# Optimization experiments

Hardware: AMD Instinct MI355X
Metric: run time of the kernel (lower is better)

## Reference

```python
import jax, jax.numpy as jnp
import numpy as np

N_NODES = 20000
DEG = 16          # neighbors per node
IN_F = 256
HEADS = 8
D_HEAD = 64       # out_features per head


def setup_inputs() -> dict:
    key = jax.random.key(0)
    k1, k2, k3 = jax.random.split(key, 3)
    x = jax.random.normal(k1, (N_NODES, IN_F), dtype=jnp.float32)
    # xavier-ish scale for params
    W = jax.random.normal(k2, (IN_F, HEADS * D_HEAD), dtype=jnp.float32) * (2.0 / (IN_F + HEADS * D_HEAD)) ** 0.5
    a = jax.random.normal(k3, (1, HEADS, 2 * D_HEAD), dtype=jnp.float32) * 0.1
    # structured edges: each node i has DEG distinct neighbors (i + j*37) % N
    # distinctness per (row, col) pair mirrors the dense attention[row, col] = e overwrite semantics
    row = jnp.repeat(jnp.arange(N_NODES, dtype=jnp.int64), DEG)
    offs = jnp.arange(1, DEG + 1, dtype=jnp.int64) * 37
    col = (row + jnp.tile(offs, N_NODES)) % N_NODES
    edge_index = jnp.stack([row, col], axis=0)
    return {"x": x, "W": W, "a": a, "edge_index": edge_index}


def _gat_forward(x, W, a, edge_index):
    N = x.shape[0]
    H = a.shape[1]
    D = a.shape[2] // 2
    h = (x @ W).reshape(N, H, D)                         # [N, H, D]
    a_src, a_dst = a[0, :, :D], a[0, :, D:]              # [H, D] each
    # e_ij = a . cat(h_i, h_j)  decomposed into per-node terms (same math)
    alpha_src = jnp.einsum('nhd,hd->nh', h, a_src)       # [N, H]
    alpha_dst = jnp.einsum('nhd,hd->nh', h, a_dst)       # [N, H]
    row, col = edge_index[0], edge_index[1]
    e = alpha_src[row] + alpha_dst[col]                  # [E, H] edge logits
    # faithful dense softmax over dim=1 of an [N, N, H] tensor whose non-edge
    # entries are 0: denominator includes (N - deg) * exp(0 - m)
    deg = jax.ops.segment_sum(jnp.ones_like(row, dtype=x.dtype), row, num_segments=N)  # [N]
    m_edge = jax.ops.segment_max(e, row, num_segments=N)                               # [N, H]
    m = jnp.maximum(m_edge, 0.0)                         # zeros participate in the max
    exp_e = jnp.exp(e - m[row])                          # [E, H]
    denom = jax.ops.segment_sum(exp_e, row, num_segments=N) \
        + (jnp.asarray(N, x.dtype) - deg)[:, None] * jnp.exp(-m)  # [N, H]
    attn = exp_e / denom[row]                            # [E, H]
    # weighted neighbor aggregation (scatter-add over destination row)
    msgs = attn[:, :, None] * h[col]                     # [E, H, D]
    out = jax.ops.segment_sum(msgs, row, num_segments=N) # [N, H, D]
    out = jax.nn.relu(out)
    return out.reshape(N, H * D)                         # concat=True


def reference(x, W, a, edge_index):
    return _gat_forward(x, W, a, edge_index)
```

## Files before the change

kernel.cpp:

```cpp
#include <hip/hip_runtime.h>
#include <hip/hip_bf16.h>

#define N_NODES 20000
#define DEG     16
#define IN_F    256
#define HEADS   8
#define D_HEAD  64
#define OUT_F   512

typedef __attribute__((ext_vector_type(8))) short bf16x8;
typedef __attribute__((ext_vector_type(4))) float f32x4;

static __device__ __forceinline__ unsigned short f2bf(float f) {
    unsigned int u = __float_as_uint(f);
    return (unsigned short)((u + 0x7fffu + ((u >> 16) & 1u)) >> 16);
}
static __device__ __forceinline__ float bf2f(unsigned short u) {
    return __uint_as_float(((unsigned int)u) << 16);
}
static __device__ __forceinline__ unsigned int pack2(float lo, float hi) {
    return (unsigned int)f2bf(lo) | ((unsigned int)f2bf(hi) << 16);
}

__global__ __launch_bounds__(256) void wconvert(const float* __restrict__ W,
                                                unsigned short* __restrict__ Wt) {
    const int k0 = blockIdx.x * 64, c0 = blockIdx.y * 64;
    const int t = threadIdx.x;
    __shared__ unsigned short lt[64][72];
    #pragma unroll
    for (int p = 0; p < 4; ++p) {
        const int r  = (t >> 4) + p * 16;
        const int cq = (t & 15) * 4;
        float4 v = *(const float4*)(W + (size_t)(k0 + r) * OUT_F + c0 + cq);
        lt[cq + 0][r] = f2bf(v.x);
        lt[cq + 1][r] = f2bf(v.y);
        lt[cq + 2][r] = f2bf(v.z);
        lt[cq + 3][r] = f2bf(v.w);
    }
    __syncthreads();
    const int c = t >> 2, q = t & 3;
    uint4 o0 = *(const uint4*)&lt[c][q * 16];
    uint4 o1 = *(const uint4*)&lt[c][q * 16 + 8];
    unsigned short* dst = Wt + (size_t)(c0 + c) * IN_F + k0 + q * 16;
    *(uint4*)dst = o0;
    *(uint4*)(dst + 8) = o1;
}

__global__ __launch_bounds__(256) void gat_gemm_mfma(
    const float* __restrict__ x, const unsigned short* __restrict__ Wt,
    const float* __restrict__ a, unsigned short* __restrict__ hbf,
    float* __restrict__ asrc, float* __restrict__ adst)
{
    int b = blockIdx.x;
    {
        const int q = 626 / 8, r = 626 % 8;
        const int xcd = b & 7, lo = b >> 3;
        b = (xcd < r ? xcd * (q + 1) : r * (q + 1) + (xcd - r) * q) + lo;
    }
    const int bx = b & 1, by = b >> 1;
    const int row0 = by * 64, col0 = bx * 256;
    const int t = threadIdx.x, w = t >> 6, l = t & 63;
    const int lr = l & 15, lk = l >> 4;
    const int head = bx * 4 + w;
    const int wcol = col0 + w * 64;

    __shared__ unsigned short xl[2][64][40];

    f32x4 acc[4][4];
    #pragma unroll
    for (int m = 0; m < 4; ++m)
        #pragma unroll
        for (int n = 0; n < 4; ++n) acc[m][n] = (f32x4)0.f;

    const int sr = t >> 2;
    const int sq = t & 3;
    const float* xrow = x + (size_t)(row0 + sr) * IN_F + sq * 8;
    const bool rok = (row0 + sr) < N_NODES;

    {
        float4 v1 = make_float4(0.f,0.f,0.f,0.f), v2 = v1;
        if (rok) { v1 = *(const float4*)xrow; v2 = *(const float4*)(xrow + 4); }
        uint4 u;
        u.x = pack2(v1.x, v1.y); u.y = pack2(v1.z, v1.w);
        u.z = pack2(v2.x, v2.y); u.w = pack2(v2.z, v2.w);
        *(uint4*)&xl[0][sr][sq * 8] = u;
    }
    __syncthreads();

    #pragma unroll 2
    for (int kt = 0; kt < 8; ++kt) {
        const int cur = kt & 1;
        float4 v1, v2;
        if (kt < 7) {
            v1 = make_float4(0.f,0.f,0.f,0.f); v2 = v1;
            if (rok) {
                v1 = *(const float4*)(xrow + (kt + 1) * 32);
                v2 = *(const float4*)(xrow + (kt + 1) * 32 + 4);
            }
        }
        bf16x8 bfrag[4], afrag[4];
        #pragma unroll
        for (int n = 0; n < 4; ++n)
            bfrag[n] = *(const bf16x8*)(Wt + (size_t)(wcol + n * 16 + lr) * IN_F
                                        + kt * 32 + lk * 8);
        #pragma unroll
        for (int m = 0; m < 4; ++m)
            afrag[m] = *(const bf16x8*)&xl[cur][m * 16 + lr][lk * 8];
        #pragma unroll
        for (int m = 0; m < 4; ++m)
            #pragma unroll
            for (int n = 0; n < 4; ++n)
                acc[m][n] = __builtin_amdgcn_mfma_f32_16x16x32_bf16(
                                afrag[m], bfrag[n], acc[m][n], 0, 0, 0);
        if (kt < 7) {
            uint4 u;
            u.x = pack2(v1.x, v1.y); u.y = pack2(v1.z, v1.w);
            u.z = pack2(v2.x, v2.y); u.w = pack2(v2.z, v2.w);
            *(uint4*)&xl[cur ^ 1][sr][sq * 8] = u;
        }
        __syncthreads();
    }

    float avs[4], avd[4];
    #pragma unroll
    for (int n = 0; n < 4; ++n) {
        avs[n] = a[head * 128 + n * 16 + lr];
        avd[n] = a[head * 128 + 64 + n * 16 + lr];
    }
    float ps[4][4], pd[4][4];
    #pragma unroll
    for (int m = 0; m < 4; ++m)
        #pragma unroll
        for (int i = 0; i < 4; ++i) {
            float s = 0.f, d = 0.f;
            #pragma unroll
            for (int n = 0; n < 4; ++n) {
                s = fmaf(acc[m][n][i], avs[n], s);
                d = fmaf(acc[m][n][i], avd[n], d);
            }
            ps[m][i] = s; pd[m][i] = d;
        }
    #pragma unroll
    for (int m = 0; m < 4; ++m)
        #pragma unroll
        for (int i = 0; i < 4; ++i) {
            const int row = row0 + m * 16 + lk * 4 + i;
            if (row < N_NODES) {
                #pragma unroll
                for (int n = 0; n < 4; ++n)
                    hbf[(size_t)row * OUT_F + wcol + n * 16 + lr] =
                        f2bf(acc[m][n][i]);
            }
        }
    #pragma unroll
    for (int mask = 1; mask < 16; mask <<= 1)
        #pragma unroll
        for (int m = 0; m < 4; ++m)
            #pragma unroll
            for (int i = 0; i < 4; ++i) {
                ps[m][i] += __shfl_xor(ps[m][i], mask);
                pd[m][i] += __shfl_xor(pd[m][i], mask);
            }
    if (lr == 0) {
        #pragma unroll
        for (int m = 0; m < 4; ++m)
            #pragma unroll
            for (int i = 0; i < 4; ++i) {
                const int row = row0 + m * 16 + lk * 4 + i;
                if (row < N_NODES) {
                    asrc[(size_t)row * HEADS + head] = ps[m][i];
                    adst[(size_t)row * HEADS + head] = pd[m][i];
                }
            }
    }
}

__global__ __launch_bounds__(256) void gat_aggregate(
    const unsigned short* __restrict__ hbf,
    const float* __restrict__ asrc, const float* __restrict__ adst,
    const int* __restrict__ col, float* __restrict__ out)
{
    int b = blockIdx.x;
    b = (b & 7) * 625 + (b >> 3);
    const int wv = threadIdx.x >> 6, l = threadIdx.x & 63;
    const int n = b * 4 + wv;
    const int j = l & 15, h0 = l >> 4;

    const int cj = col[n * DEG + j];
    const float e0 = asrc[n * HEADS + h0]     + adst[(size_t)cj * HEADS + h0];
    const float e1 = asrc[n * HEADS + h0 + 4] + adst[(size_t)cj * HEADS + h0 + 4];

    float m0 = e0, m1 = e1;
    #pragma unroll
    for (int mask = 1; mask < 16; mask <<= 1) {
        m0 = fmaxf(m0, __shfl_xor(m0, mask));
        m1 = fmaxf(m1, __shfl_xor(m1, mask));
    }
    m0 = fmaxf(m0, 0.f); m1 = fmaxf(m1, 0.f);
    const float x0 = __expf(e0 - m0), x1 = __expf(e1 - m1);
    float s0 = x0, s1 = x1;
    #pragma unroll
    for (int mask = 1; mask < 16; mask <<= 1) {
        s0 += __shfl_xor(s0, mask);
        s1 += __shfl_xor(s1, mask);
    }
    s0 += (float)(N_NODES - DEG) * __expf(-m0);
    s1 += (float)(N_NODES - DEG) * __expf(-m1);
    const float at0 = x0 / s0, at1 = x1 / s1;

    const int hme = l >> 3;
    const int slb = (hme & 3) << 4;
    const unsigned short* hbase = hbf + (size_t)l * 8;
    float a8[8];
    #pragma unroll
    for (int q = 0; q < 8; ++q) a8[q] = 0.f;
    #pragma unroll
    for (int jj = 0; jj < DEG; ++jj) {
        const int   cjj = __shfl(cj, jj);
        const float w0  = __shfl(at0, slb | jj);
        const float w1  = __shfl(at1, slb | jj);
        const float wgt = (hme < 4) ? w0 : w1;
        const uint4 v = *(const uint4*)(hbase + (size_t)cjj * OUT_F);
        a8[0] = fmaf(wgt, bf2f((unsigned short)(v.x & 0xffffu)), a8[0]);
        a8[1] = fmaf(wgt, bf2f((unsigned short)(v.x >> 16)),     a8[1]);
        a8[2] = fmaf(wgt, bf2f((unsigned short)(v.y & 0xffffu)), a8[2]);
        a8[3] = fmaf(wgt, bf2f((unsigned short)(v.y >> 16)),     a8[3]);
        a8[4] = fmaf(wgt, bf2f((unsigned short)(v.z & 0xffffu)), a8[4]);
        a8[5] = fmaf(wgt, bf2f((unsigned short)(v.z >> 16)),     a8[5]);
        a8[6] = fmaf(wgt, bf2f((unsigned short)(v.w & 0xffffu)), a8[6]);
        a8[7] = fmaf(wgt, bf2f((unsigned short)(v.w >> 16)),     a8[7]);
    }
    float4 o0, o1;
    o0.x = fmaxf(a8[0], 0.f); o0.y = fmaxf(a8[1], 0.f);
    o0.z = fmaxf(a8[2], 0.f); o0.w = fmaxf(a8[3], 0.f);
    o1.x = fmaxf(a8[4], 0.f); o1.y = fmaxf(a8[5], 0.f);
    o1.z = fmaxf(a8[6], 0.f); o1.w = fmaxf(a8[7], 0.f);
    float* op = out + (size_t)n * OUT_F + l * 8;
    *(float4*)op = o0;
    *(float4*)(op + 4) = o1;
}

extern "C" void kernel_launch(void* const* d_in, const int* in_sizes, int n_in,
                              void* d_out, int out_size, void* d_ws, size_t ws_size,
                              hipStream_t stream) {
    const float* x  = (const float*)d_in[0];
    const float* W  = (const float*)d_in[1];
    const float* a  = (const float*)d_in[2];
    const int*   ei = (const int*)d_in[3];
    const int*   colIdx = ei + (size_t)N_NODES * DEG;
    float* out = (float*)d_out;

    unsigned char* ws = (unsigned char*)d_ws;
    unsigned short* Wt  = (unsigned short*)ws;
    unsigned short* hbf = (unsigned short*)(ws + 256 * 1024);
    float* asrc = (float*)(ws + 256 * 1024 + (size_t)N_NODES * OUT_F * 2);
    float* adst = asrc + (size_t)N_NODES * HEADS;

    wconvert<<<dim3(IN_F / 64, OUT_F / 64), 256, 0, stream>>>(W, Wt);
    gat_gemm_mfma<<<626, 256, 0, stream>>>(x, Wt, a, hbf, asrc, adst);
    gat_aggregate<<<5000, 256, 0, stream>>>(hbf, asrc, adst, colIdx, out);
}
```

Before: 130.7 us.

## Widen GEMM blocks to all heads, prefetch W fragments, batch gather loads in aggregate

The GEMM kernel now uses 512-thread blocks covering all 8 heads for 64 rows, so each x tile is loaded and converted once instead of twice, and B fragments are register-prefetched one k-step ahead. The aggregate kernel has every lane load all 16 neighbor indices and issue all 16 row gathers up front, computing softmax per lane redundantly instead of through shuffles. Normalization is deferred to a single multiply at the end, and bf16 unpacking uses cheaper mask ops. This raises register pressure (16 uint4 plus weights per lane) and duplicates exp work across lanes in exchange for more memory-level parallelism.

```diff
diff --git a/kernel.cpp b/kernel.cpp
--- a/kernel.cpp
+++ b/kernel.cpp
@@ -15,8 +15,11 @@
     unsigned int u = __float_as_uint(f);
     return (unsigned short)((u + 0x7fffu + ((u >> 16) & 1u)) >> 16);
 }
-static __device__ __forceinline__ float bf2f(unsigned short u) {
-    return __uint_as_float(((unsigned int)u) << 16);
+static __device__ __forceinline__ float bf2f_lo(unsigned int v) {
+    return __uint_as_float(v << 16);
+}
+static __device__ __forceinline__ float bf2f_hi(unsigned int v) {
+    return __uint_as_float(v & 0xffff0000u);
 }
 static __device__ __forceinline__ unsigned int pack2(float lo, float hi) {
     return (unsigned int)f2bf(lo) | ((unsigned int)f2bf(hi) << 16);
@@ -46,23 +49,16 @@
     *(uint4*)(dst + 8) = o1;
 }
 
-__global__ __launch_bounds__(256) void gat_gemm_mfma(
+__global__ __launch_bounds__(512) void gat_gemm_mfma(
     const float* __restrict__ x, const unsigned short* __restrict__ Wt,
     const float* __restrict__ a, unsigned short* __restrict__ hbf,
     float* __restrict__ asrc, float* __restrict__ adst)
 {
-    int b = blockIdx.x;
-    {
-        const int q = 626 / 8, r = 626 % 8;
-        const int xcd = b & 7, lo = b >> 3;
-        b = (xcd < r ? xcd * (q + 1) : r * (q + 1) + (xcd - r) * q) + lo;
-    }
-    const int bx = b & 1, by = b >> 1;
-    const int row0 = by * 64, col0 = bx * 256;
+    const int row0 = blockIdx.x * 64;
     const int t = threadIdx.x, w = t >> 6, l = t & 63;
     const int lr = l & 15, lk = l >> 4;
-    const int head = bx * 4 + w;
-    const int wcol = col0 + w * 64;
+    const int head = w;
+    const int wcol = w * 64;
 
     __shared__ unsigned short xl[2][64][40];
 
@@ -72,37 +68,39 @@
         #pragma unroll
         for (int n = 0; n < 4; ++n) acc[m][n] = (f32x4)0.f;
 
-    const int sr = t >> 2;
-    const int sq = t & 3;
-    const float* xrow = x + (size_t)(row0 + sr) * IN_F + sq * 8;
+    const int sr = t >> 3;
+    const int sq = t & 7;
+    const float* xrow = x + (size_t)(row0 + sr) * IN_F + sq * 4;
     const bool rok = (row0 + sr) < N_NODES;
 
     {
-        float4 v1 = make_float4(0.f,0.f,0.f,0.f), v2 = v1;
-        if (rok) { v1 = *(const float4*)xrow; v2 = *(const float4*)(xrow + 4); }
-        uint4 u;
-        u.x = pack2(v1.x, v1.y); u.y = pack2(v1.z, v1.w);
-        u.z = pack2(v2.x, v2.y); u.w = pack2(v2.z, v2.w);
-        *(uint4*)&xl[0][sr][sq * 8] = u;
-    }
+        float4 v = make_float4(0.f, 0.f, 0.f, 0.f);
+        if (rok) v = *(const float4*)xrow;
+        uint2 u;
+        u.x = pack2(v.x, v.y); u.y = pack2(v.z, v.w);
+        *(uint2*)&xl[0][sr][sq * 4] = u;
+    }
+    const unsigned short* wbase = Wt + (size_t)(wcol + lr) * IN_F + lk * 8;
+    bf16x8 bcur[4];
+    #pragma unroll
+    for (int n = 0; n < 4; ++n)
+        bcur[n] = *(const bf16x8*)(wbase + (size_t)n * 16 * IN_F);
     __syncthreads();
 
     #pragma unroll 2
     for (int kt = 0; kt < 8; ++kt) {
         const int cur = kt & 1;
-        float4 v1, v2;
+        float4 v;
+        bf16x8 bnext[4];
         if (kt < 7) {
-            v1 = make_float4(0.f,0.f,0.f,0.f); v2 = v1;
-            if (rok) {
-                v1 = *(const float4*)(xrow + (kt + 1) * 32);
-                v2 = *(const float4*)(xrow + (kt + 1) * 32 + 4);
-            }
-        }
-        bf16x8 bfrag[4], afrag[4];
-        #pragma unroll
-        for (int n = 0; n < 4; ++n)
-            bfrag[n] = *(const bf16x8*)(Wt + (size_t)(wcol + n * 16 + lr) * IN_F
-                                        + kt * 32 + lk * 8);
+            v = make_float4(0.f, 0.f, 0.f, 0.f);
+            if (rok) v = *(const float4*)(xrow + (kt + 1) * 32);
+            #pragma unroll
+            for (int n = 0; n < 4; ++n)
+                bnext[n] = *(const bf16x8*)(wbase + (size_t)n * 16 * IN_F
+                                            + (kt + 1) * 32);
+        }
+        bf16x8 afrag[4];
         #pragma unroll
         for (int m = 0; m < 4; ++m)
             afrag[m] = *(const bf16x8*)&xl[cur][m * 16 + lr][lk * 8];
@@ -111,12 +109,13 @@
             #pragma unroll
             for (int n = 0; n < 4; ++n)
                 acc[m][n] = __builtin_amdgcn_mfma_f32_16x16x32_bf16(
-                                afrag[m], bfrag[n], acc[m][n], 0, 0, 0);
+                                afrag[m], bcur[n], acc[m][n], 0, 0, 0);
         if (kt < 7) {
-            uint4 u;
-            u.x = pack2(v1.x, v1.y); u.y = pack2(v1.z, v1.w);
-            u.z = pack2(v2.x, v2.y); u.w = pack2(v2.z, v2.w);
-            *(uint4*)&xl[cur ^ 1][sr][sq * 8] = u;
+            uint2 u;
+            u.x = pack2(v.x, v.y); u.y = pack2(v.z, v.w);
+            *(uint2*)&xl[cur ^ 1][sr][sq * 4] = u;
+            #pragma unroll
+            for (int n = 0; n < 4; ++n) bcur[n] = bnext[n];
         }
         __syncthreads();
     }
@@ -182,59 +181,67 @@
 {
     int b = blockIdx.x;
     b = (b & 7) * 625 + (b >> 3);
-    const int wv = threadIdx.x >> 6, l = threadIdx.x & 63;
-    const int n = b * 4 + wv;
-    const int j = l & 15, h0 = l >> 4;
-
-    const int cj = col[n * DEG + j];
-    const float e0 = asrc[n * HEADS + h0]     + adst[(size_t)cj * HEADS + h0];
-    const float e1 = asrc[n * HEADS + h0 + 4] + adst[(size_t)cj * HEADS + h0 + 4];
-
-    float m0 = e0, m1 = e1;
-    #pragma unroll
-    for (int mask = 1; mask < 16; mask <<= 1) {
-        m0 = fmaxf(m0, __shfl_xor(m0, mask));
-        m1 = fmaxf(m1, __shfl_xor(m1, mask));
-    }
-    m0 = fmaxf(m0, 0.f); m1 = fmaxf(m1, 0.f);
-    const float x0 = __expf(e0 - m0), x1 = __expf(e1 - m1);
-    float s0 = x0, s1 = x1;
-    #pragma unroll
-    for (int mask = 1; mask < 16; mask <<= 1) {
-        s0 += __shfl_xor(s0, mask);
-        s1 += __shfl_xor(s1, mask);
-    }
-    s0 += (float)(N_NODES - DEG) * __expf(-m0);
-    s1 += (float)(N_NODES - DEG) * __expf(-m1);
-    const float at0 = x0 / s0, at1 = x1 / s1;
+    const int wv = __builtin_amdgcn_readfirstlane((int)(threadIdx.x >> 6));
+    const int l  = threadIdx.x & 63;
+    const int n  = b * 4 + wv;
+
+    int sc[DEG];
+    {
+        const int4* cp = (const int4*)(col + (size_t)n * DEG);
+        #pragma unroll
+        for (int q = 0; q < 4; ++q) {
+            int4 c4 = cp[q];
+            sc[q * 4 + 0] = c4.x; sc[q * 4 + 1] = c4.y;
+            sc[q * 4 + 2] = c4.z; sc[q * 4 + 3] = c4.w;
+        }
+    }
+
+    const unsigned short* hb = hbf + (size_t)l * 8;
+    uint4 hv[DEG];
+    #pragma unroll
+    for (int jj = 0; jj < DEG; ++jj)
+        hv[jj] = *(const uint4*)(hb + (size_t)sc[jj] * OUT_F);
 
     const int hme = l >> 3;
-    const int slb = (hme & 3) << 4;
-    const unsigned short* hbase = hbf + (size_t)l * 8;
+    const float as_n = asrc[(size_t)n * HEADS + hme];
+    float e[DEG];
+    #pragma unroll
+    for (int jj = 0; jj < DEG; ++jj)
+        e[jj] = as_n + adst[(size_t)sc[jj] * HEADS + hme];
+
+    float m = 0.f;
+    #pragma unroll
+    for (int jj = 0; jj < DEG; ++jj) m = fmaxf(m, e[jj]);
+    float wgt[DEG];
+    float s = (float)(N_NODES - DEG) * __expf(-m);
+    #pragma unroll
+    for (int jj = 0; jj < DEG; ++jj) {
+        wgt[jj] = __expf(e[jj] - m);
+        s += wgt[jj];
+    }
+    const float sinv = 1.0f / s;
+
     float a8[8];
     #pragma unroll
     for (int q = 0; q < 8; ++q) a8[q] = 0.f;
     #pragma unroll
     for (int jj = 0; jj < DEG; ++jj) {
-        const int   cjj = __shfl(cj, jj);
-        const float w0  = __shfl(at0, slb | jj);
-        const float w1  = __shfl(at1, slb | jj);
-        const float wgt = (hme < 4) ? w0 : w1;
-        const uint4 v = *(const uint4*)(hbase + (size_t)cjj * OUT_F);
-        a8[0] = fmaf(wgt, bf2f((unsigned short)(v.x & 0xffffu)), a8[0]);
-        a8[1] = fmaf(wgt, bf2f((unsigned short)(v.x >> 16)),     a8[1]);
-        a8[2] = fmaf(wgt, bf2f((unsigned short)(v.y & 0xffffu)), a8[2]);
-        a8[3] = fmaf(wgt, bf2f((unsigned short)(v.y >> 16)),     a8[3]);
-        a8[4] = fmaf(wgt, bf2f((unsigned short)(v.z & 0xffffu)), a8[4]);
-        a8[5] = fmaf(wgt, bf2f((unsigned short)(v.z >> 16)),     a8[5]);
-        a8[6] = fmaf(wgt, bf2f((unsigned short)(v.w & 0xffffu)), a8[6]);
-        a8[7] = fmaf(wgt, bf2f((unsigned short)(v.w >> 16)),     a8[7]);
+        const float wg = wgt[jj];
+        const uint4 v = hv[jj];
+        a8[0] = fmaf(wg, bf2f_lo(v.x), a8[0]);
+        a8[1] = fmaf(wg, bf2f_hi(v.x), a8[1]);
+        a8[2] = fmaf(wg, bf2f_lo(v.y), a8[2]);
+        a8[3] = fmaf(wg, bf2f_hi(v.y), a8[3]);
+        a8[4] = fmaf(wg, bf2f_lo(v.z), a8[4]);
+        a8[5] = fmaf(wg, bf2f_hi(v.z), a8[5]);
+        a8[6] = fmaf(wg, bf2f_lo(v.w), a8[6]);
+        a8[7] = fmaf(wg, bf2f_hi(v.w), a8[7]);
     }
     float4 o0, o1;
-    o0.x = fmaxf(a8[0], 0.f); o0.y = fmaxf(a8[1], 0.f);
-    o0.z = fmaxf(a8[2], 0.f); o0.w = fmaxf(a8[3], 0.f);
-    o1.x = fmaxf(a8[4], 0.f); o1.y = fmaxf(a8[5], 0.f);
-    o1.z = fmaxf(a8[6], 0.f); o1.w = fmaxf(a8[7], 0.f);
+    o0.x = fmaxf(a8[0] * sinv, 0.f); o0.y = fmaxf(a8[1] * sinv, 0.f);
+    o0.z = fmaxf(a8[2] * sinv, 0.f); o0.w = fmaxf(a8[3] * sinv, 0.f);
+    o1.x = fmaxf(a8[4] * sinv, 0.f); o1.y = fmaxf(a8[5] * sinv, 0.f);
+    o1.z = fmaxf(a8[6] * sinv, 0.f); o1.w = fmaxf(a8[7] * sinv, 0.f);
     float* op = out + (size_t)n * OUT_F + l * 8;
     *(float4*)op = o0;
     *(float4*)(op + 4) = o1;
@@ -257,6 +264,6 @@
     float* adst = asrc + (size_t)N_NODES * HEADS;
 
     wconvert<<<dim3(IN_F / 64, OUT_F / 64), 256, 0, stream>>>(W, Wt);
-    gat_gemm_mfma<<<626, 256, 0, stream>>>(x, Wt, a, hbf, asrc, adst);
+    gat_gemm_mfma<<<(N_NODES + 63) / 64, 512, 0, stream>>>(x, Wt, a, hbf, asrc, adst);
     gat_aggregate<<<5000, 256, 0, stream>>>(hbf, asrc, adst, colIdx, out);
 }
```

Result: faster. 127.0 us (-2.9%).
